# Kernel optimization log

Hardware: AMD Instinct MI355X
Metric: run time of the kernel (lower is better)

The kernel has to match this reference:

```python
import jax, jax.numpy as jnp
import numpy as np

B, S, I = 4096, 128, 8
H = 512
L = 3


def setup_inputs() -> dict:
    key = jax.random.key(0)
    ks = jax.random.split(key, 5)
    scale = 1.0 / np.sqrt(H)
    return {
        "input": jax.random.normal(ks[0], (B, S, I), dtype=jnp.float32),
        "Wih": jax.random.normal(ks[1], (L, 3 * H, I), dtype=jnp.float32) * scale,
        "Whh": jax.random.normal(ks[2], (L, 3 * H, H), dtype=jnp.float32) * scale,
        "bih": jax.random.normal(ks[3], (L, 3 * H), dtype=jnp.float32) * scale,
        "bhh": jax.random.normal(ks[4], (L, 3 * H), dtype=jnp.float32) * scale,
    }


def _gru_cell(x, h, Wih, Whh, bih, bhh):
    # PyTorch GRUCell gate order: reset, update, new
    gi = x @ Wih.T + bih            # [B, 3H]
    gh = h @ Whh.T + bhh            # [B, 3H]
    i_r, i_z, i_n = jnp.split(gi, 3, axis=-1)
    h_r, h_z, h_n = jnp.split(gh, 3, axis=-1)
    r = jax.nn.sigmoid(i_r + h_r)
    z = jax.nn.sigmoid(i_z + h_z)
    n = jnp.tanh(i_n + r * h_n)
    return (1.0 - z) * n + z * h


def reference(input, Wih, Whh, bih, bhh):
    batch = input.shape[0]
    h0 = jnp.zeros((batch, Wih.shape[1] // 3), dtype=input.dtype)

    def step(h, x_t):
        # each layer consumes the same raw input x_t, chaining the context
        for l in range(Wih.shape[0]):
            h = _gru_cell(x_t, h, Wih[l], Whh[l], bih[l], bhh[l])
        return h, None

    xs = jnp.swapaxes(input, 0, 1)  # [S, B, I]
    h_final, _ = jax.lax.scan(step, h0, xs)
    return h_final
```

## Files before the change

kernel.cpp:

```cpp
#include <hip/hip_runtime.h>

typedef __attribute__((ext_vector_type(8))) short short8;
typedef __attribute__((ext_vector_type(4))) float f32x4;
typedef __attribute__((ext_vector_type(4))) int   i32x4;

#define MFMA(a,b,c)  __builtin_amdgcn_mfma_f32_16x16x32_bf16(a,b,c,0,0,0)
#define MFMAI(a,b,c) __builtin_amdgcn_mfma_i32_16x16x64_i8(a,b,c,0,0,0)

#define S_LEN 128
#define IN_D  8
#define HID   512
#define NL    3
#define H8STR 528
#define LOG2E  1.4426950408889634f
#define LOG2E2 2.8853901617779268f

#define OFF_WI8  0
#define OFF_WIH  (2359296)
#define OFF_SW   (2359296 + 294912)
#define OFF_SWI  (OFF_SW + 18432)
#define OFF_FLAG (OFF_SWI + 18432)
#define OFF_XCHG (OFF_FLAG + 1024)

__device__ __forceinline__ unsigned short f2bf(float f){
  unsigned u = __float_as_uint(f);
  u += 0x7FFFu + ((u >> 16) & 1u);
  return (unsigned short)(u >> 16);
}
__device__ __forceinline__ float fexp2(float x){ return __builtin_amdgcn_exp2f(x); }
__device__ __forceinline__ float frcp(float x){ return __builtin_amdgcn_rcpf(x); }

__global__ void prep_scale(const float* __restrict__ Whh,
                           float* __restrict__ sw, float* __restrict__ swi){
  int row = blockIdx.x * 4 + (threadIdx.x >> 6);
  int lane = threadIdx.x & 63;
  const float* src = Whh + (size_t)row * 512;
  float m = 0.f;
#pragma unroll
  for (int i = 0; i < 8; ++i) m = fmaxf(m, fabsf(src[lane + i * 64]));
#pragma unroll
  for (int off = 32; off; off >>= 1) m = fmaxf(m, (float)__shfl_xor(m, off));
  m = fmaxf(m, 1e-20f);
  if (lane == 0){ sw[row] = m / 127.f; swi[row] = 127.f / m; }
}

__global__ void prep_wi8(const float* __restrict__ Whh, const float* __restrict__ swi,
                         unsigned char* __restrict__ Wp8){
  int gid = blockIdx.x * 256 + threadIdx.x;
  int lane = gid & 63;
  int r = gid >> 6;
  int g  = r % 3;  r /= 3;
  int kk = r & 7;  r >>= 3;
  int nt = r & 31;
  int l  = r >> 5;
  int row = l * 1536 + g * 512 + nt * 16 + (lane & 15);
  int k0  = kk * 64 + (lane >> 4) * 16;
  const float* src = Whh + (size_t)row * 512 + k0;
  float si = swi[row];
  uint4 v = {0,0,0,0};
  unsigned w[4] = {0,0,0,0};
#pragma unroll
  for (int j = 0; j < 16; ++j){
    int q = (int)rintf(src[j] * si);
    q = q > 127 ? 127 : (q < -127 ? -127 : q);
    w[j >> 2] |= ((unsigned)(q & 0xFF)) << ((j & 3) * 8);
  }
  v.x = w[0]; v.y = w[1]; v.z = w[2]; v.w = w[3];
  *(uint4*)(Wp8 + (size_t)gid * 16) = v;
}

__global__ void prep_wih(const float* __restrict__ Wih, unsigned short* __restrict__ Wip){
  int gid = blockIdx.x * 256 + threadIdx.x;
  int lane = gid & 63;
  int r = gid >> 6;
  int g  = r % 3;  r /= 3;
  int nt = r & 31;
  int l  = r >> 5;
  float scl = (g == 2) ? LOG2E2 : LOG2E;
  unsigned short t[8] = {0,0,0,0,0,0,0,0};
  if ((lane >> 4) == 0){
    int n = g * 512 + nt * 16 + (lane & 15);
    const float* src = Wih + ((size_t)l * 1536 + n) * 8;
#pragma unroll
    for (int j = 0; j < 8; ++j) t[j] = f2bf(src[j] * scl);
  }
  uint4 v;
  v.x = t[0] | ((unsigned)t[1] << 16);
  v.y = t[2] | ((unsigned)t[3] << 16);
  v.z = t[4] | ((unsigned)t[5] << 16);
  v.w = t[6] | ((unsigned)t[7] << 16);
  *(uint4*)(Wip + (size_t)gid * 8) = v;
}

__global__ __launch_bounds__(1024) void gru_main(
    const float* __restrict__ x,
    const unsigned char* __restrict__ Wp8,
    const unsigned short* __restrict__ Wip,
    const float* __restrict__ bih,
    const float* __restrict__ bhh,
    const float* __restrict__ sw,
    float* __restrict__ out,
    int* __restrict__ flags,
    unsigned int* __restrict__ xchg)
{
  __shared__ __align__(16) unsigned char  hB8[2][32 * H8STR];
  __shared__ __align__(16) unsigned short xpack[2][1024];
  __shared__ __align__(16) float sBrz[3 * 1024];
  __shared__ __align__(16) float sBni[3 * 512];
  __shared__ __align__(16) float sBnh[3 * 512];
  __shared__ __align__(16) float sK[4608];
  __shared__ int   pad[1024];

  const int tid  = threadIdx.x;
  const int wv   = tid >> 6;
  const int lane = tid & 63;
  const int l15  = lane & 15;
  const int l4   = lane >> 4;

  const int bid     = blockIdx.x;
  const int bgroup  = ((bid >> 3) << 2) | (bid & 3);
  const int half    = (bid >> 2) & 1;
  const int partner = bid ^ 4;
  const int b0      = bgroup * 32;
  const int colv    = half * 256 + wv * 16 + l4 * 4;
  const int ntc     = half * 16 + wv;
  const int pcb0    = (1 - half) * 256;
  const int ko0     = half * 4;
  const int pk0     = 4 - ko0;

  if (flags[bid] == -1) pad[tid] = tid;

  unsigned int* xown = xchg + (size_t)bid * 4096;
  const unsigned int* xpb = xchg + (size_t)partner * 4096 + tid;
  const int dOff = (tid >> 6) * H8STR + pcb0 + (tid & 63) * 4;

  for (int i = tid; i < 2 * 32 * H8STR / 4; i += 1024) ((unsigned*)hB8)[i] = 0;
  for (int i = tid; i < 3072; i += 1024){
    int l = i >> 10, c = i & 1023;
    sBrz[i] = (bih[l * 1536 + c] + bhh[l * 1536 + c]) * LOG2E;
  }
  for (int i = tid; i < 1536; i += 1024){
    int l = i >> 9, c = i & 511;
    sBni[i] = bih[l * 1536 + 1024 + c] * LOG2E2;
    sBnh[i] = bhh[l * 1536 + 1024 + c] * LOG2E2;
  }
  for (int i = tid; i < 4608; i += 1024){
    int g = (i % 1536) >> 9;
    sK[i] = sw[i] * (1.f / 127.f) * (g == 2 ? LOG2E2 : LOG2E);
  }

  float hreg[2][4];
#pragma unroll
  for (int nf = 0; nf < 2; ++nf)
#pragma unroll
    for (int q = 0; q < 4; ++q) hreg[nf][q] = 0.f;

  const int xl = (tid >> 3) & 63;
  const size_t xbase = ((size_t)(b0 + (tid >> 9) * 16 + (xl & 15))) * (S_LEN * IN_D) + (tid & 7);
  const int xvalid = (xl < 16);
  { float xv = xvalid ? x[xbase] : 0.f; xpack[0][tid] = f2bf(xv); }
  __syncthreads();

  const int boff0 = l15 * H8STR + l4 * 16;
  const int boff1 = boff0 + 16 * H8STR;

  const unsigned char*  wklB = Wp8 + (size_t)ntc * (8 * 3 * 64 * 16) + (size_t)lane * 16;
  const unsigned short* wilB = Wip + (size_t)ntc * 3 * 512 + (size_t)lane * 8;

#define DO_KK(kkv) { \
    const int kk_ = (kkv); \
    const unsigned char* w_ = wkl + kk_ * 3072; \
    i32x4 wR = *(const i32x4*)(w_); \
    i32x4 wZ = *(const i32x4*)(w_ + 1024); \
    i32x4 wN = *(const i32x4*)(w_ + 2048); \
    i32x4 hb0 = *(const i32x4*)(hb8c + boff0 + kk_ * 64); \
    i32x4 hb1 = *(const i32x4*)(hb8c + boff1 + kk_ * 64); \
    aR[0] = MFMAI(wR, hb0, aR[0]);  aR[1] = MFMAI(wR, hb1, aR[1]); \
    aZ[0] = MFMAI(wZ, hb0, aZ[0]);  aZ[1] = MFMAI(wZ, hb1, aZ[1]); \
    aN[0] = MFMAI(wN, hb0, aN[0]);  aN[1] = MFMAI(wN, hb1, aN[1]); \
  }

  int cur = 0;
#pragma unroll 1
  for (int t = 0; t < S_LEN; ++t){
    const unsigned short* xp = &xpack[t & 1][0];
#pragma unroll 1
    for (int l = 0; l < NL; ++l){
      const int s    = t * NL + l;
      const int last = (s == S_LEN * NL - 1);
      const unsigned char* hb8c = hB8[cur];
      unsigned char*       hb8w = hB8[cur];
      unsigned char*       hb8n = hB8[cur ^ 1];
      const unsigned char*  wkl = wklB + (size_t)l * (32 * 8 * 3 * 64 * 16);
      const unsigned short* wil = wilB + (size_t)l * (32 * 3 * 512);

      unsigned c0 = 0, c1 = 0;
      if (s > 0){
        while (__hip_atomic_load(&flags[partner], __ATOMIC_RELAXED, __HIP_MEMORY_SCOPE_AGENT) < s)
          __builtin_amdgcn_s_sleep(4);
        const unsigned int* src = xpb + ((s - 1) & 1) * 2048;
        c0 = __hip_atomic_load(src,        __ATOMIC_RELAXED, __HIP_MEMORY_SCOPE_AGENT);
        c1 = __hip_atomic_load(src + 1024, __ATOMIC_RELAXED, __HIP_MEMORY_SCOPE_AGENT);
      }

      const f32x4 vR4  = *(const f32x4*)&sBrz[l * 1024 + colv];
      const f32x4 vZ4  = *(const f32x4*)&sBrz[l * 1024 + 512 + colv];
      const f32x4 vNi4 = *(const f32x4*)&sBni[l * 512 + colv];
      const f32x4 vNh4 = *(const f32x4*)&sBnh[l * 512 + colv];
      const f32x4 kR4  = *(const f32x4*)&sK[l * 1536 + colv];
      const f32x4 kZ4  = *(const f32x4*)&sK[l * 1536 + 512 + colv];
      const f32x4 kN4  = *(const f32x4*)&sK[l * 1536 + 1024 + colv];

      f32x4 gR[2], gZ[2], gN[2];
      gR[0] = vR4;  gR[1] = vR4;
      gZ[0] = vZ4;  gZ[1] = vZ4;
      gN[0] = vNi4; gN[1] = vNi4;

      {
        short8 wiR = *(const short8*)(wil);
        short8 wiZ = *(const short8*)(wil + 512);
        short8 wiN = *(const short8*)(wil + 1024);
        short8 xb0 = *(const short8*)(xp + lane * 8);
        short8 xb1 = *(const short8*)(xp + 512 + lane * 8);
        gR[0] = MFMA(wiR, xb0, gR[0]);  gR[1] = MFMA(wiR, xb1, gR[1]);
        gZ[0] = MFMA(wiZ, xb0, gZ[0]);  gZ[1] = MFMA(wiZ, xb1, gZ[1]);
        gN[0] = MFMA(wiN, xb0, gN[0]);  gN[1] = MFMA(wiN, xb1, gN[1]);
      }

      i32x4 aR[2], aZ[2], aN[2];
#pragma unroll
      for (int nf = 0; nf < 2; ++nf){
        aR[nf] = (i32x4){0,0,0,0};
        aZ[nf] = (i32x4){0,0,0,0};
        aN[nf] = (i32x4){0,0,0,0};
      }

#pragma unroll
      for (int kx = 0; kx < 4; ++kx) DO_KK(ko0 + kx);

      if (s > 0){
        *(unsigned*)(hb8w + dOff)              = c0;
        *(unsigned*)(hb8w + dOff + 16 * H8STR) = c1;
      }
      __syncthreads();

#pragma unroll
      for (int kx = 0; kx < 4; ++kx) DO_KK(pk0 + kx);

      unsigned int* xob = xown + (s & 1) * 2048;
#pragma unroll
      for (int nf = 0; nf < 2; ++nf){
        unsigned pk = 0;
#pragma unroll
        for (int q = 0; q < 4; ++q){
          float rp = gR[nf][q] + (float)aR[nf][q] * kR4[q];
          float zp = gZ[nf][q] + (float)aZ[nf][q] * kZ4[q];
          float r  = frcp(1.f + fexp2(-rp));
          float z  = frcp(1.f + fexp2(-zp));
          float an = gN[nf][q] + r * ((float)aN[nf][q] * kN4[q] + vNh4[q]);
          float n  = fmaf(-2.f, frcp(1.f + fexp2(an)), 1.f);
          float hn = fmaf(z, hreg[nf][q] - n, n);
          hreg[nf][q] = hn;
          int hq = (int)rintf(hn * 127.f);
          pk |= ((unsigned)(hq & 0xFF)) << (q * 8);
        }
        int brow = nf * 16 + l15;
        *(unsigned*)(hb8n + brow * H8STR + colv) = pk;
        if (!last)
          __hip_atomic_store(xob + brow * 64 + wv * 4 + l4, pk,
                             __ATOMIC_RELAXED, __HIP_MEMORY_SCOPE_AGENT);
      }

      if (l == NL - 1 && t < S_LEN - 1){
        float xv = xvalid ? x[xbase + (size_t)(t + 1) * IN_D] : 0.f;
        xpack[(t + 1) & 1][tid] = f2bf(xv);
      }

      if (!last){
        asm volatile("s_waitcnt vmcnt(0)" ::: "memory");
        __syncthreads();
        if (tid == 0)
          __hip_atomic_store(&flags[bid], s + 1, __ATOMIC_RELAXED, __HIP_MEMORY_SCOPE_AGENT);
      }
      cur ^= 1;
    }
  }
#undef DO_KK

#pragma unroll
  for (int nf = 0; nf < 2; ++nf){
    f32x4 v = { hreg[nf][0], hreg[nf][1], hreg[nf][2], hreg[nf][3] };
    int brow = nf * 16 + l15;
    *(f32x4*)&out[((size_t)(b0 + brow)) * 512 + colv] = v;
  }

  if (flags[bid] == -2) out[0] = (float)pad[tid];
}

extern "C" void kernel_launch(void* const* d_in, const int* in_sizes, int n_in,
                              void* d_out, int out_size, void* d_ws, size_t ws_size,
                              hipStream_t stream){
  const float* x   = (const float*)d_in[0];
  const float* Wih = (const float*)d_in[1];
  const float* Whh = (const float*)d_in[2];
  const float* bih = (const float*)d_in[3];
  const float* bhh = (const float*)d_in[4];

  unsigned char* ws = (unsigned char*)d_ws;
  unsigned char*  Wp8  = (unsigned char*)(ws + OFF_WI8);
  unsigned short* Wip  = (unsigned short*)(ws + OFF_WIH);
  float*          sw   = (float*)(ws + OFF_SW);
  float*          swi  = (float*)(ws + OFF_SWI);
  int*            flg  = (int*)(ws + OFF_FLAG);
  unsigned int*   xchg = (unsigned int*)(ws + OFF_XCHG);

  hipMemsetAsync(flg, 0, 256 * sizeof(int), stream);
  prep_scale<<<1152, 256, 0, stream>>>(Whh, sw, swi);
  prep_wi8  <<< 576, 256, 0, stream>>>(Whh, swi, Wp8);
  prep_wih  <<<  72, 256, 0, stream>>>(Wih, Wip);
  gru_main  <<< 256, 1024, 0, stream>>>(x, Wp8, Wip, bih, bhh, sw, (float*)d_out, flg, xchg);
}
```

Before: 2.837 ms.

## Split each batch group's hidden columns across four cooperating blocks instead of two

Each 32-row batch group is now handled by four blocks of 512 threads, one per 128-column quarter of the hidden state, instead of two blocks of 1024 threads. Blocks trade quantized hidden slices with three siblings through global memory, with flag polling on all three. The aim is to spread the recurrent matmul over 512 workgroups to use more CUs and give each wave fewer MFMAs per step. In exchange, every step pays more cross-block synchronisation and global exchange traffic, and a slow sibling stalls the others.

```diff
diff --git a/kernel.cpp b/kernel.cpp
--- a/kernel.cpp
+++ b/kernel.cpp
@@ -20,7 +20,7 @@
 #define OFF_SW   (2359296 + 294912)
 #define OFF_SWI  (OFF_SW + 18432)
 #define OFF_FLAG (OFF_SWI + 18432)
-#define OFF_XCHG (OFF_FLAG + 1024)
+#define OFF_XCHG (OFF_FLAG + 2048)
 
 __device__ __forceinline__ unsigned short f2bf(float f){
   unsigned u = __float_as_uint(f);
@@ -92,7 +92,7 @@
   *(uint4*)(Wip + (size_t)gid * 8) = v;
 }
 
-__global__ __launch_bounds__(1024) void gru_main(
+__global__ __launch_bounds__(512, 4) void gru_main(
     const float* __restrict__ x,
     const unsigned char* __restrict__ Wp8,
     const unsigned short* __restrict__ Wip,
@@ -105,11 +105,11 @@
 {
   __shared__ __align__(16) unsigned char  hB8[2][32 * H8STR];
   __shared__ __align__(16) unsigned short xpack[2][1024];
-  __shared__ __align__(16) float sBrz[3 * 1024];
-  __shared__ __align__(16) float sBni[3 * 512];
-  __shared__ __align__(16) float sBnh[3 * 512];
-  __shared__ __align__(16) float sK[4608];
-  __shared__ int   pad[1024];
+  __shared__ __align__(16) float sBrz[3 * 256];
+  __shared__ __align__(16) float sBni[3 * 128];
+  __shared__ __align__(16) float sBnh[3 * 128];
+  __shared__ __align__(16) float sK[3 * 384];
+  __shared__ int   pad[1536];
 
   const int tid  = threadIdx.x;
   const int wv   = tid >> 6;
@@ -117,48 +117,56 @@
   const int l15  = lane & 15;
   const int l4   = lane >> 4;
 
-  const int bid     = blockIdx.x;
-  const int bgroup  = ((bid >> 3) << 2) | (bid & 3);
-  const int half    = (bid >> 2) & 1;
-  const int partner = bid ^ 4;
-  const int b0      = bgroup * 32;
-  const int colv    = half * 256 + wv * 16 + l4 * 4;
-  const int ntc     = half * 16 + wv;
-  const int pcb0    = (1 - half) * 256;
-  const int ko0     = half * 4;
-  const int pk0     = 4 - ko0;
+  const int bid  = blockIdx.x;
+  const int q    = bid & 3;
+  const int sib  = bid & ~3;
+  const int b0   = (bid >> 2) * 32;
+  const int lc   = wv * 16 + l4 * 4;
+  const int colv = q * 128 + lc;
+  const int ntc  = q * 8 + wv;
 
   if (flags[bid] == -1) pad[tid] = tid;
 
-  unsigned int* xown = xchg + (size_t)bid * 4096;
-  const unsigned int* xpb = xchg + (size_t)partner * 4096 + tid;
-  const int dOff = (tid >> 6) * H8STR + pcb0 + (tid & 63) * 4;
-
-  for (int i = tid; i < 2 * 32 * H8STR / 4; i += 1024) ((unsigned*)hB8)[i] = 0;
-  for (int i = tid; i < 3072; i += 1024){
-    int l = i >> 10, c = i & 1023;
-    sBrz[i] = (bih[l * 1536 + c] + bhh[l * 1536 + c]) * LOG2E;
-  }
-  for (int i = tid; i < 1536; i += 1024){
-    int l = i >> 9, c = i & 511;
-    sBni[i] = bih[l * 1536 + 1024 + c] * LOG2E2;
-    sBnh[i] = bhh[l * 1536 + 1024 + c] * LOG2E2;
-  }
-  for (int i = tid; i < 4608; i += 1024){
-    int g = (i % 1536) >> 9;
-    sK[i] = sw[i] * (1.f / 127.f) * (g == 2 ? LOG2E2 : LOG2E);
+  const int q1 = (q + 1) & 3, q2 = (q + 2) & 3, q3 = (q + 3) & 3;
+  unsigned int* xown = xchg + (size_t)bid * 2048;
+  const unsigned int* p0 = xchg + (size_t)(sib | q1) * 2048 + tid;
+  const unsigned int* p1 = xchg + (size_t)(sib | q2) * 2048 + tid;
+  const unsigned int* p2 = xchg + (size_t)(sib | q3) * 2048 + tid;
+  const int dbase = (tid >> 5) * H8STR + (tid & 31) * 4;
+  const int d0 = dbase + q1 * 128, d1 = dbase + q2 * 128, d2 = dbase + q3 * 128;
+
+  for (int i = tid; i < 2 * 32 * H8STR / 4; i += 512) ((unsigned*)hB8)[i] = 0;
+  for (int i = tid; i < 768; i += 512){
+    int l = i >> 8, c = i & 255;
+    int gc = l * 1536 + ((c < 128) ? (q * 128 + c) : (512 + q * 128 + (c - 128)));
+    sBrz[i] = (bih[gc] + bhh[gc]) * LOG2E;
+  }
+  if (tid < 384){
+    int l = tid >> 7, c = tid & 127;
+    int gc = l * 1536 + 1024 + q * 128 + c;
+    sBni[tid] = bih[gc] * LOG2E2;
+    sBnh[tid] = bhh[gc] * LOG2E2;
+  }
+  for (int i = tid; i < 1152; i += 512){
+    int l = i / 384, rem = i % 384, g = rem >> 7, c = rem & 127;
+    int row = l * 1536 + g * 512 + q * 128 + c;
+    sK[i] = sw[row] * (1.f / 127.f) * (g == 2 ? LOG2E2 : LOG2E);
   }
 
   float hreg[2][4];
 #pragma unroll
   for (int nf = 0; nf < 2; ++nf)
 #pragma unroll
-    for (int q = 0; q < 4; ++q) hreg[nf][q] = 0.f;
+    for (int qq = 0; qq < 4; ++qq) hreg[nf][qq] = 0.f;
 
   const int xl = (tid >> 3) & 63;
-  const size_t xbase = ((size_t)(b0 + (tid >> 9) * 16 + (xl & 15))) * (S_LEN * IN_D) + (tid & 7);
+  const size_t xbase  = ((size_t)(b0 + (xl & 15))) * (S_LEN * IN_D) + (tid & 7);
+  const size_t xbase2 = xbase + (size_t)16 * (S_LEN * IN_D);
   const int xvalid = (xl < 16);
-  { float xv = xvalid ? x[xbase] : 0.f; xpack[0][tid] = f2bf(xv); }
+  {
+    xpack[0][tid]       = f2bf(xvalid ? x[xbase]  : 0.f);
+    xpack[0][tid + 512] = f2bf(xvalid ? x[xbase2] : 0.f);
+  }
   __syncthreads();
 
   const int boff0 = l15 * H8STR + l4 * 16;
@@ -194,22 +202,31 @@
       const unsigned char*  wkl = wklB + (size_t)l * (32 * 8 * 3 * 64 * 16);
       const unsigned short* wil = wilB + (size_t)l * (32 * 3 * 512);
 
-      unsigned c0 = 0, c1 = 0;
+      unsigned ca0=0, ca1=0, cb0=0, cb1=0, cc0=0, cc1=0;
       if (s > 0){
-        while (__hip_atomic_load(&flags[partner], __ATOMIC_RELAXED, __HIP_MEMORY_SCOPE_AGENT) < s)
+        for (;;){
+          int f1 = __hip_atomic_load(&flags[sib | q1], __ATOMIC_RELAXED, __HIP_MEMORY_SCOPE_AGENT);
+          int f2 = __hip_atomic_load(&flags[sib | q2], __ATOMIC_RELAXED, __HIP_MEMORY_SCOPE_AGENT);
+          int f3 = __hip_atomic_load(&flags[sib | q3], __ATOMIC_RELAXED, __HIP_MEMORY_SCOPE_AGENT);
+          if (f1 >= s && f2 >= s && f3 >= s) break;
           __builtin_amdgcn_s_sleep(4);
-        const unsigned int* src = xpb + ((s - 1) & 1) * 2048;
-        c0 = __hip_atomic_load(src,        __ATOMIC_RELAXED, __HIP_MEMORY_SCOPE_AGENT);
-        c1 = __hip_atomic_load(src + 1024, __ATOMIC_RELAXED, __HIP_MEMORY_SCOPE_AGENT);
-      }
-
-      const f32x4 vR4  = *(const f32x4*)&sBrz[l * 1024 + colv];
-      const f32x4 vZ4  = *(const f32x4*)&sBrz[l * 1024 + 512 + colv];
-      const f32x4 vNi4 = *(const f32x4*)&sBni[l * 512 + colv];
-      const f32x4 vNh4 = *(const f32x4*)&sBnh[l * 512 + colv];
-      const f32x4 kR4  = *(const f32x4*)&sK[l * 1536 + colv];
-      const f32x4 kZ4  = *(const f32x4*)&sK[l * 1536 + 512 + colv];
-      const f32x4 kN4  = *(const f32x4*)&sK[l * 1536 + 1024 + colv];
+        }
+        const int so = ((s - 1) & 1) * 1024;
+        ca0 = __hip_atomic_load(p0 + so,       __ATOMIC_RELAXED, __HIP_MEMORY_SCOPE_AGENT);
+        ca1 = __hip_atomic_load(p0 + so + 512, __ATOMIC_RELAXED, __HIP_MEMORY_SCOPE_AGENT);
+        cb0 = __hip_atomic_load(p1 + so,       __ATOMIC_RELAXED, __HIP_MEMORY_SCOPE_AGENT);
+        cb1 = __hip_atomic_load(p1 + so + 512, __ATOMIC_RELAXED, __HIP_MEMORY_SCOPE_AGENT);
+        cc0 = __hip_atomic_load(p2 + so,       __ATOMIC_RELAXED, __HIP_MEMORY_SCOPE_AGENT);
+        cc1 = __hip_atomic_load(p2 + so + 512, __ATOMIC_RELAXED, __HIP_MEMORY_SCOPE_AGENT);
+      }
+
+      const f32x4 vR4  = *(const f32x4*)&sBrz[l * 256 + lc];
+      const f32x4 vZ4  = *(const f32x4*)&sBrz[l * 256 + 128 + lc];
+      const f32x4 vNi4 = *(const f32x4*)&sBni[l * 128 + lc];
+      const f32x4 vNh4 = *(const f32x4*)&sBnh[l * 128 + lc];
+      const f32x4 kR4  = *(const f32x4*)&sK[l * 384 + lc];
+      const f32x4 kZ4  = *(const f32x4*)&sK[l * 384 + 128 + lc];
+      const f32x4 kN4  = *(const f32x4*)&sK[l * 384 + 256 + lc];
 
       f32x4 gR[2], gZ[2], gN[2];
       gR[0] = vR4;  gR[1] = vR4;
@@ -235,45 +252,50 @@
         aN[nf] = (i32x4){0,0,0,0};
       }
 
-#pragma unroll
-      for (int kx = 0; kx < 4; ++kx) DO_KK(ko0 + kx);
+      DO_KK(q * 2);
+      DO_KK(q * 2 + 1);
 
       if (s > 0){
-        *(unsigned*)(hb8w + dOff)              = c0;
-        *(unsigned*)(hb8w + dOff + 16 * H8STR) = c1;
+        *(unsigned*)(hb8w + d0)              = ca0;
+        *(unsigned*)(hb8w + d0 + 16 * H8STR) = ca1;
+        *(unsigned*)(hb8w + d1)              = cb0;
+        *(unsigned*)(hb8w + d1 + 16 * H8STR) = cb1;
+        *(unsigned*)(hb8w + d2)              = cc0;
+        *(unsigned*)(hb8w + d2 + 16 * H8STR) = cc1;
       }
       __syncthreads();
 
-#pragma unroll
-      for (int kx = 0; kx < 4; ++kx) DO_KK(pk0 + kx);
-
-      unsigned int* xob = xown + (s & 1) * 2048;
+      DO_KK(q1 * 2);  DO_KK(q1 * 2 + 1);
+      DO_KK(q2 * 2);  DO_KK(q2 * 2 + 1);
+      DO_KK(q3 * 2);  DO_KK(q3 * 2 + 1);
+
+      unsigned int* xob = xown + (s & 1) * 1024;
 #pragma unroll
       for (int nf = 0; nf < 2; ++nf){
         unsigned pk = 0;
 #pragma unroll
-        for (int q = 0; q < 4; ++q){
-          float rp = gR[nf][q] + (float)aR[nf][q] * kR4[q];
-          float zp = gZ[nf][q] + (float)aZ[nf][q] * kZ4[q];
+        for (int qq = 0; qq < 4; ++qq){
+          float rp = gR[nf][qq] + (float)aR[nf][qq] * kR4[qq];
+          float zp = gZ[nf][qq] + (float)aZ[nf][qq] * kZ4[qq];
           float r  = frcp(1.f + fexp2(-rp));
           float z  = frcp(1.f + fexp2(-zp));
-          float an = gN[nf][q] + r * ((float)aN[nf][q] * kN4[q] + vNh4[q]);
+          float an = gN[nf][qq] + r * ((float)aN[nf][qq] * kN4[qq] + vNh4[qq]);
           float n  = fmaf(-2.f, frcp(1.f + fexp2(an)), 1.f);
-          float hn = fmaf(z, hreg[nf][q] - n, n);
-          hreg[nf][q] = hn;
+          float hn = fmaf(z, hreg[nf][qq] - n, n);
+          hreg[nf][qq] = hn;
           int hq = (int)rintf(hn * 127.f);
-          pk |= ((unsigned)(hq & 0xFF)) << (q * 8);
+          pk |= ((unsigned)(hq & 0xFF)) << (qq * 8);
         }
         int brow = nf * 16 + l15;
         *(unsigned*)(hb8n + brow * H8STR + colv) = pk;
         if (!last)
-          __hip_atomic_store(xob + brow * 64 + wv * 4 + l4, pk,
+          __hip_atomic_store(xob + brow * 32 + wv * 4 + l4, pk,
                              __ATOMIC_RELAXED, __HIP_MEMORY_SCOPE_AGENT);
       }
 
       if (l == NL - 1 && t < S_LEN - 1){
-        float xv = xvalid ? x[xbase + (size_t)(t + 1) * IN_D] : 0.f;
-        xpack[(t + 1) & 1][tid] = f2bf(xv);
+        xpack[(t + 1) & 1][tid]       = f2bf(xvalid ? x[xbase  + (size_t)(t + 1) * IN_D] : 0.f);
+        xpack[(t + 1) & 1][tid + 512] = f2bf(xvalid ? x[xbase2 + (size_t)(t + 1) * IN_D] : 0.f);
       }
 
       if (!last){
@@ -314,9 +336,9 @@
   int*            flg  = (int*)(ws + OFF_FLAG);
   unsigned int*   xchg = (unsigned int*)(ws + OFF_XCHG);
 
-  hipMemsetAsync(flg, 0, 256 * sizeof(int), stream);
+  hipMemsetAsync(flg, 0, 512 * sizeof(int), stream);
   prep_scale<<<1152, 256, 0, stream>>>(Whh, sw, swi);
   prep_wi8  <<< 576, 256, 0, stream>>>(Whh, swi, Wp8);
   prep_wih  <<<  72, 256, 0, stream>>>(Wih, Wip);
-  gru_main  <<< 256, 1024, 0, stream>>>(x, Wp8, Wip, bih, bhh, sw, (float*)d_out, flg, xchg);
-}
+  gru_main  <<< 512, 512, 0, stream>>>(x, Wp8, Wip, bih, bhh, sw, (float*)d_out, flg, xchg);
+}
```

New measurement: 4.217 ms. 1.49x slower.
